# Kernel tuning notes

Measured on AMD Instinct MI355X. Metric: run time of the kernel, lower is better.

## Reference

```python
import jax, jax.numpy as jnp
import numpy as np

B, C, H, E, V = 64, 200, 1024, 1024, 50257
NEG_INF = -100000.0


def setup_inputs() -> dict:
    key = jax.random.key(0)
    ks = jax.random.split(key, 16)
    p = 1.0 / np.sqrt(H)
    inp = {
        "input": jax.random.normal(ks[0], (B, 1, E), jnp.float32),
        "hidden": jax.random.normal(ks[1], (1, B, H), jnp.float32),
        "list_context_hidden": jax.random.normal(ks[2], (C, B, H), jnp.float32),
        "context_hiddens": jax.random.normal(ks[3], (B, C, H), jnp.float32),
        "topic_vector": jax.random.normal(ks[4], (B, 1, H), jnp.float32),
        "pad_matrix": jax.random.randint(ks[5], (B, C), 0, 2) > 0,
        # attention params
        "dyna_W": jax.random.normal(ks[6], (H, H), jnp.float32) * p,
        "dyna_U": jax.random.normal(ks[7], (H, H), jnp.float32) * p,
        "dyna_v": jax.random.normal(ks[8], (H, 1), jnp.float32) * p,
        # GRU params (torch layout: W_ih (3H, in), W_hh (3H, H))
        "W_ih": jax.random.normal(ks[9], (3 * H, 2 * H + E), jnp.float32) * p,
        "W_hh": jax.random.normal(ks[10], (3 * H, H), jnp.float32) * p,
        "b_ih": jax.random.normal(ks[11], (3 * H,), jnp.float32) * p,
        "b_hh": jax.random.normal(ks[12], (3 * H,), jnp.float32) * p,
        # output projection
        "W_out": jax.random.normal(ks[13], (V, H), jnp.float32) * p,
        "b_out": jax.random.normal(ks[14], (V,), jnp.float32) * p,
    }
    return inp


def _gru_step(x, h, W_ih, W_hh, b_ih, b_hh):
    # x: (B, in), h: (B, H) -> h': (B, H); torch GRUCell math
    gi = x @ W_ih.T + b_ih            # (B, 3H)
    gh = h @ W_hh.T + b_hh            # (B, 3H)
    r = jax.nn.sigmoid(gi[:, :H] + gh[:, :H])
    z = jax.nn.sigmoid(gi[:, H:2 * H] + gh[:, H:2 * H])
    n = jnp.tanh(gi[:, 2 * H:] + r * gh[:, 2 * H:])
    return (1.0 - z) * n + z * h


def reference(input, hidden, list_context_hidden, context_hiddens, topic_vector,
              pad_matrix, dyna_W, dyna_U, dyna_v, W_ih, W_hh, b_ih, b_hh,
              W_out, b_out):
    h0 = hidden[0]                                         # (B, H)
    # additive attention, vectorized over the C contexts
    q = h0 @ dyna_W                                        # (B, H)
    k = jnp.einsum('cbh,hk->cbk', list_context_hidden, dyna_U)  # (C, B, H)
    scores = jnp.tanh(q[None, :, :] + k) @ dyna_v          # (C, B, 1)
    scores = scores[..., 0].T                              # (B, C)
    scores = jnp.where(pad_matrix, NEG_INF, scores)
    attn = jax.nn.softmax(scores, axis=1)                  # (B, C)
    applied = jnp.einsum('bc,bch->bh', attn, context_hiddens)  # (B, H)
    # GRU over a single step
    x = jnp.concatenate([input[:, 0], topic_vector[:, 0], applied], axis=1)  # (B, E+2H)
    h_new = _gru_step(x, h0, W_ih, W_hh, b_ih, b_hh)       # (B, H)
    logits = h_new @ W_out.T + b_out                       # (B, V)
    out = jax.nn.log_softmax(logits, axis=1)
    return out, h_new[None]
```

## Files before the change

kernel.cpp:

```cpp
#include <hip/hip_runtime.h>
#include <hip/hip_bf16.h>
#include <math.h>

constexpr int Bsz = 64, Cctx = 200, Hdim = 1024, Vv = 50257;
constexpr float NEG_INF_V = -100000.0f;

typedef __attribute__((ext_vector_type(8))) short s16x8;
typedef __attribute__((ext_vector_type(4))) float fx4;
typedef unsigned int u32;

__device__ __forceinline__ unsigned short f2bf(float f) {
  unsigned int u = __builtin_bit_cast(unsigned int, f);
  unsigned int r = (u + 0x7fffu + ((u >> 16) & 1u)) >> 16;
  return (unsigned short)r;
}

__device__ __forceinline__ float fast_tanh(float x) {
  float e2 = __expf(2.f * x);
  return 1.f - 2.f / (e2 + 1.f);
}

__device__ __forceinline__ void gl_lds16(const unsigned short* g, unsigned short* l) {
  __builtin_amdgcn_global_load_lds(
      (const __attribute__((address_space(1))) u32*)g,
      (__attribute__((address_space(3))) u32*)l, 16, 0, 0);
}

__global__ __launch_bounds__(256)
void gemm_att(const unsigned short* __restrict__ Ab, const unsigned short* __restrict__ Bb,
              const float* __restrict__ qmat, const float* __restrict__ vvec,
              float* __restrict__ part_sc) {
  __shared__ unsigned short As[128 * 64];
  __shared__ unsigned short Bs[64 * 64];
  const int bx = blockIdx.x, by = blockIdx.y;
  const int xcd = bx;
  const int my = xcd + 8 * (by >> 4);
  const int mx = by & 15;
  if (my >= 100) return;
  const int bm0 = my * 128, bn0 = mx * 64;
  const int tid = threadIdx.x, lane = tid & 63, wid = tid >> 6;
  const int wm0 = wid * 32;
  const int ar = lane & 15, q4 = lane >> 4;
  const int sw = ar & 7;

  fx4 acc[2][4] = {};

  for (int t = 0; t < 16; ++t) {
    const int kt = t * 64;
    #pragma unroll
    for (int i = 0; i < 4; ++i) {
      int s = tid + i * 256;
      int row = s >> 3;
      int sc = ((s & 7) ^ (row & 7)) * 8;
      gl_lds16(&Ab[(size_t)(bm0 + row) * Hdim + kt + sc], &As[s * 8]);
    }
    #pragma unroll
    for (int i = 0; i < 2; ++i) {
      int s = tid + i * 256;
      int row = s >> 3;
      int sc = ((s & 7) ^ (row & 7)) * 8;
      gl_lds16(&Bb[(size_t)(bn0 + row) * Hdim + kt + sc], &Bs[s * 8]);
    }
    __syncthreads();
    #pragma unroll
    for (int kk = 0; kk < 2; ++kk) {
      s16x8 a[2], b[4];
      #pragma unroll
      for (int i = 0; i < 2; ++i)
        a[i] = *reinterpret_cast<const s16x8*>(
            &As[(wm0 + i * 16 + ar) * 64 + (((kk * 4 + q4) ^ sw) * 8)]);
      #pragma unroll
      for (int j2 = 0; j2 < 4; ++j2)
        b[j2] = *reinterpret_cast<const s16x8*>(
            &Bs[(j2 * 16 + ar) * 64 + (((kk * 4 + q4) ^ sw) * 8)]);
      #pragma unroll
      for (int i = 0; i < 2; ++i)
        #pragma unroll
        for (int j2 = 0; j2 < 4; ++j2)
          acc[i][j2] = __builtin_amdgcn_mfma_f32_16x16x32_bf16(a[i], b[j2], acc[i][j2], 0, 0, 0);
    }
    __syncthreads();
  }

  const int rg = q4 * 4, cg = ar;
  #pragma unroll
  for (int i = 0; i < 2; ++i) {
    #pragma unroll
    for (int p = 0; p < 4; ++p) {
      int mg = bm0 + wm0 + i * 16 + rg + p;
      int brow = mg & 63;
      float rs = 0.f;
      #pragma unroll
      for (int j2 = 0; j2 < 4; ++j2) {
        int ng = bn0 + j2 * 16 + cg;
        float t = fast_tanh(acc[i][j2][p] + qmat[brow * Hdim + ng]);
        rs += t * vvec[ng];
      }
      rs += __shfl_xor(rs, 1); rs += __shfl_xor(rs, 2);
      rs += __shfl_xor(rs, 4); rs += __shfl_xor(rs, 8);
      if (cg == 0) part_sc[mx * 12800 + brow * Cctx + (mg >> 6)] = rs;
    }
  }
}

__device__ __forceinline__ void stream_body(const unsigned short* ap, const float* bp,
                                            int stride, int extent, fx4 acc[4]) {
  float4 b0 = *reinterpret_cast<const float4*>(bp);
  float4 b1 = *reinterpret_cast<const float4*>(bp + 4);
  float4 b2 = *reinterpret_cast<const float4*>(bp + 32);
  float4 b3 = *reinterpret_cast<const float4*>(bp + 36);
  for (int kt = 0; kt < extent; kt += 64) {
    float4 c0 = b0, c1 = b1, c2 = b2, c3 = b3;
    if (kt + 64 < extent) {
      b0 = *reinterpret_cast<const float4*>(bp + kt + 64);
      b1 = *reinterpret_cast<const float4*>(bp + kt + 68);
      b2 = *reinterpret_cast<const float4*>(bp + kt + 96);
      b3 = *reinterpret_cast<const float4*>(bp + kt + 100);
    }
    s16x8 bf0, bf1;
    bf0[0] = (short)f2bf(c0.x); bf0[1] = (short)f2bf(c0.y);
    bf0[2] = (short)f2bf(c0.z); bf0[3] = (short)f2bf(c0.w);
    bf0[4] = (short)f2bf(c1.x); bf0[5] = (short)f2bf(c1.y);
    bf0[6] = (short)f2bf(c1.z); bf0[7] = (short)f2bf(c1.w);
    bf1[0] = (short)f2bf(c2.x); bf1[1] = (short)f2bf(c2.y);
    bf1[2] = (short)f2bf(c2.z); bf1[3] = (short)f2bf(c2.w);
    bf1[4] = (short)f2bf(c3.x); bf1[5] = (short)f2bf(c3.y);
    bf1[6] = (short)f2bf(c3.z); bf1[7] = (short)f2bf(c3.w);
    #pragma unroll
    for (int i = 0; i < 4; ++i) {
      s16x8 af = *reinterpret_cast<const s16x8*>(ap + (size_t)i * 16 * stride + kt);
      acc[i] = __builtin_amdgcn_mfma_f32_16x16x32_bf16(af, bf0, acc[i], 0, 0, 0);
    }
    #pragma unroll
    for (int i = 0; i < 4; ++i) {
      s16x8 af = *reinterpret_cast<const s16x8*>(ap + (size_t)i * 16 * stride + kt + 32);
      acc[i] = __builtin_amdgcn_mfma_f32_16x16x32_bf16(af, bf1, acc[i], 0, 0, 0);
    }
  }
}

template<int EPI>
__global__ __launch_bounds__(64)
void stream_gemm(const unsigned short* __restrict__ Ab,
                 const float* __restrict__ Bm, int N, int K,
                 const float* __restrict__ bias, float* __restrict__ Cout) {
  const int lane = threadIdx.x;
  const int n0 = blockIdx.x * 16;
  const int c = lane & 15, qq = lane >> 4;
  const int brow = min(n0 + c, N - 1);
  fx4 acc[4] = {};
  stream_body(Ab + (size_t)c * K + qq * 8, Bm + (size_t)brow * K + qq * 8, K, K, acc);
  const int n = n0 + c;
  if (n < N) {
    float bv = (EPI == 2) ? bias[n] : 0.f;
    #pragma unroll
    for (int i = 0; i < 4; ++i)
      #pragma unroll
      for (int p = 0; p < 4; ++p)
        Cout[(size_t)(i * 16 + qq * 4 + p) * N + n] = acc[i][p] + bv;
  }
}

__global__ __launch_bounds__(64)
void qgh_gemm(const unsigned short* __restrict__ h0b, const float* __restrict__ Wt,
              const float* __restrict__ Whh, const float* __restrict__ bhh,
              float* __restrict__ q, float* __restrict__ gh) {
  const int lane = threadIdx.x;
  const int gw = blockIdx.x;
  const bool isq = gw < 64;
  const int n0 = isq ? gw * 16 : (gw - 64) * 16;
  const int N = isq ? 1024 : 3072;
  const float* B = isq ? Wt : Whh;
  const int c = lane & 15, qq = lane >> 4;
  fx4 acc[4] = {};
  stream_body(h0b + (size_t)c * 1024 + qq * 8, B + (size_t)(n0 + c) * 1024 + qq * 8,
              1024, 1024, acc);
  const int n = n0 + c;
  float bv = isq ? 0.f : bhh[n];
  float* C = isq ? q : gh;
  #pragma unroll
  for (int i = 0; i < 4; ++i)
    #pragma unroll
    for (int p = 0; p < 4; ++p)
      C[(size_t)(i * 16 + qq * 4 + p) * N + n] = acc[i][p] + bv;
}

__global__ __launch_bounds__(64)
void gi_split(const unsigned short* __restrict__ xb, const float* __restrict__ Wih,
              float* __restrict__ part) {
  const int lane = threadIdx.x;
  const int t = blockIdx.x;
  const int w = blockIdx.y;
  const int c = lane & 15, qq = lane >> 4;
  constexpr int K = 3072, CH = 768;
  fx4 acc[4] = {};
  stream_body(xb + (size_t)c * K + w * CH + qq * 8,
              Wih + (size_t)(t * 16 + c) * K + w * CH + qq * 8, K, CH, acc);
  float* po = part + (size_t)w * 64 * 3072;
  const int n = t * 16 + c;
  #pragma unroll
  for (int i = 0; i < 4; ++i)
    #pragma unroll
    for (int p = 0; p < 4; ++p)
      po[(size_t)(i * 16 + qq * 4 + p) * 3072 + n] = acc[i][p];
}

__global__ __launch_bounds__(256)
void prep(const float* __restrict__ dW, const float* __restrict__ dU,
          const float* __restrict__ h0, float* __restrict__ Wt,
          unsigned short* __restrict__ ub, unsigned short* __restrict__ h0b) {
  const int z = blockIdx.z;
  const int tx = threadIdx.x & 31, ty = threadIdx.x >> 5;
  if (z < 2) {
    __shared__ float t[32][33];
    const float* in = z ? dU : dW;
    int bx = blockIdx.x * 32, by = blockIdx.y * 32;
    #pragma unroll
    for (int r = 0; r < 32; r += 8) t[ty + r][tx] = in[(size_t)(by + ty + r) * 1024 + bx + tx];
    __syncthreads();
    if (z == 0) {
      #pragma unroll
      for (int r = 0; r < 32; r += 8) Wt[(size_t)(bx + ty + r) * 1024 + by + tx] = t[tx][ty + r];
    } else {
      #pragma unroll
      for (int r = 0; r < 32; r += 8) ub[(size_t)(bx + ty + r) * 1024 + by + tx] = f2bf(t[tx][ty + r]);
    }
  } else {
    if (blockIdx.y) return;
    size_t i = (size_t)(blockIdx.x * 256 + threadIdx.x) * 8;
    float4 a = *reinterpret_cast<const float4*>(h0 + i);
    float4 b = *reinterpret_cast<const float4*>(h0 + i + 4);
    s16x8 h;
    h[0] = (short)f2bf(a.x); h[1] = (short)f2bf(a.y); h[2] = (short)f2bf(a.z); h[3] = (short)f2bf(a.w);
    h[4] = (short)f2bf(b.x); h[5] = (short)f2bf(b.y); h[6] = (short)f2bf(b.z); h[7] = (short)f2bf(b.w);
    *reinterpret_cast<s16x8*>(h0b + i) = h;
  }
}

__global__ void conv_bf16(const float* __restrict__ in, unsigned short* __restrict__ out) {
  size_t i = (size_t)(blockIdx.x * 256 + threadIdx.x) * 8;
  float4 a = *reinterpret_cast<const float4*>(in + i);
  float4 b = *reinterpret_cast<const float4*>(in + i + 4);
  s16x8 h;
  h[0] = (short)f2bf(a.x); h[1] = (short)f2bf(a.y); h[2] = (short)f2bf(a.z); h[3] = (short)f2bf(a.w);
  h[4] = (short)f2bf(b.x); h[5] = (short)f2bf(b.y); h[6] = (short)f2bf(b.z); h[7] = (short)f2bf(b.w);
  *reinterpret_cast<s16x8*>(out + i) = h;
}

__global__ __launch_bounds__(256)
void softmax_applied(const float* __restrict__ part_sc, const int* __restrict__ pad,
                     const float* __restrict__ ch, float* __restrict__ part) {
  const int g = blockIdx.x, b = blockIdx.y, t = threadIdx.x;
  const int lane = t & 63, w = t >> 6;
  __shared__ float at[256];
  __shared__ float red[8];
  float sv = 0.f, v = -3.4e38f;
  if (t < Cctx) {
    float s8 = 0.f;
    #pragma unroll
    for (int mx = 0; mx < 16; ++mx) s8 += part_sc[mx * 12800 + b * Cctx + t];
    sv = pad[b * Cctx + t] ? NEG_INF_V : s8;
    v = sv;
  }
  #pragma unroll
  for (int o = 1; o < 64; o <<= 1) v = fmaxf(v, __shfl_xor(v, o));
  if (lane == 0) red[w] = v;
  __syncthreads();
  float m = fmaxf(fmaxf(red[0], red[1]), fmaxf(red[2], red[3]));
  float e = (t < Cctx) ? expf(sv - m) : 0.f;
  float s = e;
  #pragma unroll
  for (int o = 1; o < 64; o <<= 1) s += __shfl_xor(s, o);
  if (lane == 0) red[4 + w] = s;
  __syncthreads();
  float tot = red[4] + red[5] + red[6] + red[7];
  at[t] = e / tot;
  __syncthreads();
  const int h = t * 4;
  float4 a4 = make_float4(0.f, 0.f, 0.f, 0.f);
  for (int c2 = g * 25; c2 < g * 25 + 25; ++c2) {
    float a = at[c2];
    float4 vv = *reinterpret_cast<const float4*>(&ch[((size_t)b * Cctx + c2) * Hdim + h]);
    a4.x += a * vv.x; a4.y += a * vv.y; a4.z += a * vv.z; a4.w += a * vv.w;
  }
  *reinterpret_cast<float4*>(&part[((size_t)b * 8 + g) * Hdim + h]) = a4;
}

__global__ void build_xb(const float* __restrict__ inp, const float* __restrict__ topic,
                         const float* __restrict__ part, unsigned short* __restrict__ xb) {
  int j = blockIdx.x * 256 + threadIdx.x;
  int b = blockIdx.y;
  float v;
  if (j < 1024) v = inp[b * 1024 + j];
  else if (j < 2048) v = topic[b * 1024 + (j - 1024)];
  else {
    const float* pp = &part[(size_t)b * 8 * Hdim + (j - 2048)];
    v = 0.f;
    #pragma unroll
    for (int g = 0; g < 8; ++g) v += pp[g * Hdim];
  }
  xb[(size_t)b * 3072 + j] = f2bf(v);
}

__global__ void gru_gate(const float* __restrict__ pgi, const float* __restrict__ bih,
                         const float* __restrict__ gh, const float* __restrict__ h0,
                         float* __restrict__ out_h, unsigned short* __restrict__ hnb) {
  int idx = blockIdx.x * 256 + threadIdx.x;
  int b = idx >> 10, j = idx & 1023;
  float gr = bih[j], gz = bih[1024 + j], gn = bih[2048 + j];
  const float* pb = pgi + (size_t)b * 3072;
  #pragma unroll
  for (int w = 0; w < 4; ++w) {
    const float* pw = pb + (size_t)w * 64 * 3072;
    gr += pw[j]; gz += pw[1024 + j]; gn += pw[2048 + j];
  }
  const float* ghb = gh + (size_t)b * 3072;
  float r = 1.f / (1.f + expf(-(gr + ghb[j])));
  float z = 1.f / (1.f + expf(-(gz + ghb[1024 + j])));
  float n = tanhf(gn + r * ghb[2048 + j]);
  float h = (1.f - z) * n + z * h0[idx];
  out_h[idx] = h;
  hnb[idx] = f2bf(h);
}

__global__ __launch_bounds__(1024)
void lse_fused(float* __restrict__ out) {
  const int b = blockIdx.x, t = threadIdx.x, lane = t & 63, w = t >> 6;
  __shared__ float red[16];
  float* row = out + (size_t)b * Vv;
  float m = -3.4e38f;
  for (int i = t; i < Vv; i += 1024) m = fmaxf(m, row[i]);
  #pragma unroll
  for (int o = 1; o < 64; o <<= 1) m = fmaxf(m, __shfl_xor(m, o));
  if (lane == 0) red[w] = m;
  __syncthreads();
  float mm = red[0];
  #pragma unroll
  for (int k = 1; k < 16; ++k) mm = fmaxf(mm, red[k]);
  float s = 0.f;
  for (int i = t; i < Vv; i += 1024) s += expf(row[i] - mm);
  #pragma unroll
  for (int o = 1; o < 64; o <<= 1) s += __shfl_xor(s, o);
  __syncthreads();
  if (lane == 0) red[w] = s;
  __syncthreads();
  float ss = 0.f;
  #pragma unroll
  for (int k = 0; k < 16; ++k) ss += red[k];
  float lse = mm + logf(ss);
  for (int i = t; i < Vv; i += 1024) row[i] -= lse;
}

extern "C" void kernel_launch(void* const* d_in, const int* in_sizes, int n_in,
                              void* d_out, int out_size, void* d_ws, size_t ws_size,
                              hipStream_t stream) {
  const float* input  = (const float*)d_in[0];
  const float* hidden = (const float*)d_in[1];
  const float* lch    = (const float*)d_in[2];
  const float* ch     = (const float*)d_in[3];
  const float* topic  = (const float*)d_in[4];
  const int*   pad    = (const int*)d_in[5];
  const float* dyna_W = (const float*)d_in[6];
  const float* dyna_U = (const float*)d_in[7];
  const float* dyna_v = (const float*)d_in[8];
  const float* W_ih   = (const float*)d_in[9];
  const float* W_hh   = (const float*)d_in[10];
  const float* b_ih   = (const float*)d_in[11];
  const float* b_hh   = (const float*)d_in[12];
  const float* W_out  = (const float*)d_in[13];
  const float* b_out  = (const float*)d_in[14];

  float* out   = (float*)d_out;
  float* out_h = out + (size_t)Bsz * Vv;

  float* p = (float*)d_ws;
  float* Wt      = p; p += 1024 * 1024;
  float* q       = p; p += Bsz * Hdim;
  float* part_sc = p; p += 16 * Bsz * Cctx;
  float* part_ap = p; p += Bsz * 8 * Hdim;
  float* gh      = p; p += Bsz * 3072;
  float* part_gi = p; p += 4 * Bsz * 3072;
  unsigned short* up = (unsigned short*)p;
  unsigned short* ub  = up; up += 1024 * 1024;
  unsigned short* lb  = up; up += (size_t)Cctx * Bsz * Hdim;
  unsigned short* h0b = up; up += Bsz * Hdim;
  unsigned short* hnb = up; up += Bsz * Hdim;
  unsigned short* xb  = up; up += Bsz * 3072;

  prep<<<dim3(32, 32, 3), 256, 0, stream>>>(dyna_W, dyna_U, hidden, Wt, ub, h0b);
  conv_bf16<<<(Cctx * Bsz * Hdim) / 2048, 256, 0, stream>>>(lch, lb);

  qgh_gemm<<<256, 64, 0, stream>>>(h0b, Wt, W_hh, b_hh, q, gh);

  gemm_att<<<dim3(8, 208), 256, 0, stream>>>(lb, ub, q, dyna_v, part_sc);

  softmax_applied<<<dim3(8, Bsz), 256, 0, stream>>>(part_sc, pad, ch, part_ap);
  build_xb<<<dim3(12, Bsz), 256, 0, stream>>>(input, topic, part_ap, xb);

  gi_split<<<dim3(192, 4), 64, 0, stream>>>(xb, W_ih, part_gi);

  gru_gate<<<(Bsz * Hdim) / 256, 256, 0, stream>>>(part_gi, b_ih, gh, hidden, out_h, hnb);

  stream_gemm<2><<<(Vv + 15) / 16, 64, 0, stream>>>(hnb, W_out, Vv, Hdim, b_out, out);

  lse_fused<<<Bsz, 1024, 0, stream>>>(out);
}
```

Measured before the change: 223.7 us.

## Fuse per-tile max/sum-exp into logits GEMM and merge prep launches

The logits GEMM epilogue now computes a per-16-column block max and sum of exponentials for each row and writes these partials out. A small combine kernel reduces them into a per-row log-sum-exp, and a fully parallel subtract kernel applies it. This replaces the old 64-block log-softmax kernel, which made two extra read passes over the large logits matrix with little parallelism. Separately, the prep and bf16 conversion kernels are merged into a single launch; the cost is more shuffles and partial-buffer writes in the GEMM epilogue.

```diff
diff --git a/kernel.cpp b/kernel.cpp
--- a/kernel.cpp
+++ b/kernel.cpp
@@ -3,6 +3,7 @@
 #include <math.h>
 
 constexpr int Bsz = 64, Cctx = 200, Hdim = 1024, Vv = 50257;
+constexpr int NBLK = (Vv + 15) / 16;
 constexpr float NEG_INF_V = -100000.0f;
 
 typedef __attribute__((ext_vector_type(8))) short s16x8;
@@ -139,26 +140,69 @@
   }
 }
 
-template<int EPI>
 __global__ __launch_bounds__(64)
-void stream_gemm(const unsigned short* __restrict__ Ab,
-                 const float* __restrict__ Bm, int N, int K,
-                 const float* __restrict__ bias, float* __restrict__ Cout) {
+void logits_gemm(const unsigned short* __restrict__ Ab, const float* __restrict__ Bm,
+                 const float* __restrict__ bias, float* __restrict__ Cout,
+                 float* __restrict__ pm, float* __restrict__ ps) {
   const int lane = threadIdx.x;
   const int n0 = blockIdx.x * 16;
   const int c = lane & 15, qq = lane >> 4;
-  const int brow = min(n0 + c, N - 1);
+  const int brow = min(n0 + c, Vv - 1);
   fx4 acc[4] = {};
-  stream_body(Ab + (size_t)c * K + qq * 8, Bm + (size_t)brow * K + qq * 8, K, K, acc);
+  stream_body(Ab + (size_t)c * Hdim + qq * 8, Bm + (size_t)brow * Hdim + qq * 8,
+              Hdim, Hdim, acc);
   const int n = n0 + c;
-  if (n < N) {
-    float bv = (EPI == 2) ? bias[n] : 0.f;
-    #pragma unroll
-    for (int i = 0; i < 4; ++i)
-      #pragma unroll
-      for (int p = 0; p < 4; ++p)
-        Cout[(size_t)(i * 16 + qq * 4 + p) * N + n] = acc[i][p] + bv;
-  }
+  const bool valid = n < Vv;
+  float bv = valid ? bias[n] : 0.f;
+  #pragma unroll
+  for (int i = 0; i < 4; ++i) {
+    #pragma unroll
+    for (int p = 0; p < 4; ++p) {
+      int row = i * 16 + qq * 4 + p;
+      float val = acc[i][p] + bv;
+      if (valid) Cout[(size_t)row * Vv + n] = val;
+      float mv = valid ? val : -3.4e38f;
+      mv = fmaxf(mv, __shfl_xor(mv, 1)); mv = fmaxf(mv, __shfl_xor(mv, 2));
+      mv = fmaxf(mv, __shfl_xor(mv, 4)); mv = fmaxf(mv, __shfl_xor(mv, 8));
+      float e = valid ? expf(val - mv) : 0.f;
+      e += __shfl_xor(e, 1); e += __shfl_xor(e, 2);
+      e += __shfl_xor(e, 4); e += __shfl_xor(e, 8);
+      if (c == 0) {
+        pm[(size_t)row * NBLK + blockIdx.x] = mv;
+        ps[(size_t)row * NBLK + blockIdx.x] = e;
+      }
+    }
+  }
+}
+
+__global__ __launch_bounds__(256)
+void lse_combine(const float* __restrict__ pm, const float* __restrict__ ps,
+                 float* __restrict__ lse) {
+  const int b = blockIdx.x, t = threadIdx.x, lane = t & 63, w = t >> 6;
+  __shared__ float red[8];
+  const float* pmb = pm + (size_t)b * NBLK;
+  const float* psb = ps + (size_t)b * NBLK;
+  float m = -3.4e38f;
+  for (int i = t; i < NBLK; i += 256) m = fmaxf(m, pmb[i]);
+  #pragma unroll
+  for (int o = 1; o < 64; o <<= 1) m = fmaxf(m, __shfl_xor(m, o));
+  if (lane == 0) red[w] = m;
+  __syncthreads();
+  float M = fmaxf(fmaxf(red[0], red[1]), fmaxf(red[2], red[3]));
+  float s = 0.f;
+  for (int i = t; i < NBLK; i += 256) s += psb[i] * expf(pmb[i] - M);
+  #pragma unroll
+  for (int o = 1; o < 64; o <<= 1) s += __shfl_xor(s, o);
+  if (lane == 0) red[4 + w] = s;
+  __syncthreads();
+  if (t == 0) lse[b] = M + logf(red[4] + red[5] + red[6] + red[7]);
+}
+
+__global__ __launch_bounds__(256)
+void lse_sub(float* __restrict__ out, const float* __restrict__ lse) {
+  const int b = blockIdx.y;
+  int i = blockIdx.x * 256 + threadIdx.x;
+  if (i < Vv) out[(size_t)b * Vv + i] -= lse[b];
 }
 
 __global__ __launch_bounds__(64)
@@ -206,45 +250,46 @@
 }
 
 __global__ __launch_bounds__(256)
-void prep(const float* __restrict__ dW, const float* __restrict__ dU,
-          const float* __restrict__ h0, float* __restrict__ Wt,
-          unsigned short* __restrict__ ub, unsigned short* __restrict__ h0b) {
-  const int z = blockIdx.z;
-  const int tx = threadIdx.x & 31, ty = threadIdx.x >> 5;
-  if (z < 2) {
+void prep_all(const float* __restrict__ dW, const float* __restrict__ dU,
+              const float* __restrict__ h0, const float* __restrict__ lch,
+              float* __restrict__ Wt, unsigned short* __restrict__ ub,
+              unsigned short* __restrict__ h0b, unsigned short* __restrict__ lb) {
+  const int bid = blockIdx.x;
+  const int tid = threadIdx.x;
+  if (bid < 2048) {
     __shared__ float t[32][33];
-    const float* in = z ? dU : dW;
-    int bx = blockIdx.x * 32, by = blockIdx.y * 32;
+    const int zb = bid >> 10;
+    const int t2 = bid & 1023;
+    const int bx = (t2 & 31) * 32, by = (t2 >> 5) * 32;
+    const int tx = tid & 31, ty = tid >> 5;
+    const float* in = zb ? dU : dW;
     #pragma unroll
     for (int r = 0; r < 32; r += 8) t[ty + r][tx] = in[(size_t)(by + ty + r) * 1024 + bx + tx];
     __syncthreads();
-    if (z == 0) {
+    if (zb == 0) {
       #pragma unroll
       for (int r = 0; r < 32; r += 8) Wt[(size_t)(bx + ty + r) * 1024 + by + tx] = t[tx][ty + r];
     } else {
       #pragma unroll
       for (int r = 0; r < 32; r += 8) ub[(size_t)(bx + ty + r) * 1024 + by + tx] = f2bf(t[tx][ty + r]);
     }
-  } else {
-    if (blockIdx.y) return;
-    size_t i = (size_t)(blockIdx.x * 256 + threadIdx.x) * 8;
+  } else if (bid < 2080) {
+    size_t i = (size_t)((bid - 2048) * 256 + tid) * 8;
     float4 a = *reinterpret_cast<const float4*>(h0 + i);
     float4 b = *reinterpret_cast<const float4*>(h0 + i + 4);
     s16x8 h;
     h[0] = (short)f2bf(a.x); h[1] = (short)f2bf(a.y); h[2] = (short)f2bf(a.z); h[3] = (short)f2bf(a.w);
     h[4] = (short)f2bf(b.x); h[5] = (short)f2bf(b.y); h[6] = (short)f2bf(b.z); h[7] = (short)f2bf(b.w);
     *reinterpret_cast<s16x8*>(h0b + i) = h;
-  }
-}
-
-__global__ void conv_bf16(const float* __restrict__ in, unsigned short* __restrict__ out) {
-  size_t i = (size_t)(blockIdx.x * 256 + threadIdx.x) * 8;
-  float4 a = *reinterpret_cast<const float4*>(in + i);
-  float4 b = *reinterpret_cast<const float4*>(in + i + 4);
-  s16x8 h;
-  h[0] = (short)f2bf(a.x); h[1] = (short)f2bf(a.y); h[2] = (short)f2bf(a.z); h[3] = (short)f2bf(a.w);
-  h[4] = (short)f2bf(b.x); h[5] = (short)f2bf(b.y); h[6] = (short)f2bf(b.z); h[7] = (short)f2bf(b.w);
-  *reinterpret_cast<s16x8*>(out + i) = h;
+  } else {
+    size_t i = (size_t)((bid - 2080) * 256 + tid) * 8;
+    float4 a = *reinterpret_cast<const float4*>(lch + i);
+    float4 b = *reinterpret_cast<const float4*>(lch + i + 4);
+    s16x8 h;
+    h[0] = (short)f2bf(a.x); h[1] = (short)f2bf(a.y); h[2] = (short)f2bf(a.z); h[3] = (short)f2bf(a.w);
+    h[4] = (short)f2bf(b.x); h[5] = (short)f2bf(b.y); h[6] = (short)f2bf(b.z); h[7] = (short)f2bf(b.w);
+    *reinterpret_cast<s16x8*>(lb + i) = h;
+  }
 }
 
 __global__ __launch_bounds__(256)
@@ -321,34 +366,6 @@
   float h = (1.f - z) * n + z * h0[idx];
   out_h[idx] = h;
   hnb[idx] = f2bf(h);
-}
-
-__global__ __launch_bounds__(1024)
-void lse_fused(float* __restrict__ out) {
-  const int b = blockIdx.x, t = threadIdx.x, lane = t & 63, w = t >> 6;
-  __shared__ float red[16];
-  float* row = out + (size_t)b * Vv;
-  float m = -3.4e38f;
-  for (int i = t; i < Vv; i += 1024) m = fmaxf(m, row[i]);
-  #pragma unroll
-  for (int o = 1; o < 64; o <<= 1) m = fmaxf(m, __shfl_xor(m, o));
-  if (lane == 0) red[w] = m;
-  __syncthreads();
-  float mm = red[0];
-  #pragma unroll
-  for (int k = 1; k < 16; ++k) mm = fmaxf(mm, red[k]);
-  float s = 0.f;
-  for (int i = t; i < Vv; i += 1024) s += expf(row[i] - mm);
-  #pragma unroll
-  for (int o = 1; o < 64; o <<= 1) s += __shfl_xor(s, o);
-  __syncthreads();
-  if (lane == 0) red[w] = s;
-  __syncthreads();
-  float ss = 0.f;
-  #pragma unroll
-  for (int k = 0; k < 16; ++k) ss += red[k];
-  float lse = mm + logf(ss);
-  for (int i = t; i < Vv; i += 1024) row[i] -= lse;
 }
 
 extern "C" void kernel_launch(void* const* d_in, const int* in_sizes, int n_in,
@@ -380,6 +397,9 @@
   float* part_ap = p; p += Bsz * 8 * Hdim;
   float* gh      = p; p += Bsz * 3072;
   float* part_gi = p; p += 4 * Bsz * 3072;
+  float* pm      = p; p += (size_t)Bsz * NBLK;
+  float* ps      = p; p += (size_t)Bsz * NBLK;
+  float* lse     = p; p += Bsz;
   unsigned short* up = (unsigned short*)p;
   unsigned short* ub  = up; up += 1024 * 1024;
   unsigned short* lb  = up; up += (size_t)Cctx * Bsz * Hdim;
@@ -387,8 +407,7 @@
   unsigned short* hnb = up; up += Bsz * Hdim;
   unsigned short* xb  = up; up += Bsz * 3072;
 
-  prep<<<dim3(32, 32, 3), 256, 0, stream>>>(dyna_W, dyna_U, hidden, Wt, ub, h0b);
-  conv_bf16<<<(Cctx * Bsz * Hdim) / 2048, 256, 0, stream>>>(lch, lb);
+  prep_all<<<8480, 256, 0, stream>>>(dyna_W, dyna_U, hidden, lch, Wt, ub, h0b, lb);
 
   qgh_gemm<<<256, 64, 0, stream>>>(h0b, Wt, W_hh, b_hh, q, gh);
 
@@ -401,7 +420,8 @@
 
   gru_gate<<<(Bsz * Hdim) / 256, 256, 0, stream>>>(part_gi, b_ih, gh, hidden, out_h, hnb);
 
-  stream_gemm<2><<<(Vv + 15) / 16, 64, 0, stream>>>(hnb, W_out, Vv, Hdim, b_out, out);
-
-  lse_fused<<<Bsz, 1024, 0, stream>>>(out);
-}
+  logits_gemm<<<NBLK, 64, 0, stream>>>(hnb, W_out, b_out, out, pm, ps);
+
+  lse_combine<<<Bsz, 256, 0, stream>>>(pm, ps, lse);
+  lse_sub<<<dim3((Vv + 255) / 256, Bsz), 256, 0, stream>>>(out, lse);
+}
```

Result: no change. 221.5 us (-1.0%).
